# Kernel optimization log

Hardware: AMD Instinct MI355X
Metric: run time of the kernel (lower is better)

The kernel has to match this reference:

```python
import jax, jax.numpy as jnp
import numpy as np

N = 100000
F_IN = 512
HID = 16
N_CLS = 40
E = 3200000


def gcn_conv(x, W, b, src, dst, n_nodes):
    # PyG GCNConv: add self loops, symmetric deg^{-1/2} norm, linear, aggregate.
    loop = jnp.arange(n_nodes, dtype=src.dtype)
    s = jnp.concatenate([src, loop])  # [E+N]
    d = jnp.concatenate([dst, loop])
    deg = jax.ops.segment_sum(jnp.ones_like(d, dtype=x.dtype), d, num_segments=n_nodes)
    dinv = jnp.where(deg > 0, jax.lax.rsqrt(deg), 0.0)
    norm = dinv[s] * dinv[d]  # [E+N]
    h = x @ W  # [N, out] -- transform before propagate (cheaper: out <= in)
    msg = h[s] * norm[:, None]  # gather + scale
    out = jax.ops.segment_sum(msg, d, num_segments=n_nodes)  # scatter-add
    return out + b


def setup_inputs() -> dict:
    key = jax.random.key(0)
    ks = jax.random.split(key, 6)
    x = jax.random.normal(ks[0], (N, F_IN), dtype=jnp.float32)
    edge_index = jax.random.randint(ks[1], (2, E), 0, N, dtype=jnp.int64)
    W1 = jax.random.normal(ks[2], (F_IN, HID), dtype=jnp.float32) / np.sqrt(F_IN)
    b1 = jnp.zeros((HID,), dtype=jnp.float32)
    W2 = jax.random.normal(ks[3], (HID, N_CLS), dtype=jnp.float32) / np.sqrt(HID)
    b2 = jnp.zeros((N_CLS,), dtype=jnp.float32)
    return {"x": x, "edge_index": edge_index, "W1": W1, "b1": b1, "W2": W2, "b2": b2}


def reference(x, edge_index, W1, b1, W2, b2):
    src, dst = edge_index[0], edge_index[1]
    h = gcn_conv(x, W1, b1, src, dst, x.shape[0])
    h = jax.nn.relu(h)
    # dropout: eval mode (identity) for a deterministic reference
    h = gcn_conv(h, W2, b2, src, dst, x.shape[0])
    return jax.nn.log_softmax(h, axis=1)
```

## Files before the change

### kernel.cpp

```cpp
#include <hip/hip_runtime.h>

#define N_NODES 100000
#define NEDGE   3200000
#define F_IN    512
#define HID     16
#define NCLS    40

#define BSHIFT  8
#define BNODES  256
#define NBUCK   ((N_NODES + BNODES - 1) / BNODES)
#define BCAP    8832
#define EPB     5120
#define NPART   (NEDGE / EPB)
#define NGEMM   ((N_NODES + 63) / 64)

typedef __bf16 bf16x8 __attribute__((ext_vector_type(8)));
typedef float floatx4 __attribute__((ext_vector_type(4)));
typedef _Float16 f16x4 __attribute__((ext_vector_type(4)));

__global__ __launch_bounds__(256) void k_partgemm(
        const int* __restrict__ src, const int* __restrict__ dst,
        int* __restrict__ gcnt, int* __restrict__ ebuf,
        const float* __restrict__ x, const float* __restrict__ W1,
        _Float16* __restrict__ h1u) {
    __shared__ char smraw[32768];
    int t = threadIdx.x;

    if (blockIdx.x < NPART) {
        int* hist = (int*)smraw;
        for (int i = t; i < NBUCK; i += 256) hist[i] = 0;
        __syncthreads();

        int base = blockIdx.x * EPB + t * 4;
        int4 dr[5];
        #pragma unroll
        for (int s = 0; s < 5; s++) {
            dr[s] = *(const int4*)(dst + base + s * 1024);
            atomicAdd(&hist[dr[s].x >> BSHIFT], 1);
            atomicAdd(&hist[dr[s].y >> BSHIFT], 1);
            atomicAdd(&hist[dr[s].z >> BSHIFT], 1);
            atomicAdd(&hist[dr[s].w >> BSHIFT], 1);
        }
        __syncthreads();

        for (int i = t; i < NBUCK; i += 256) {
            int h = hist[i];
            hist[i] = h ? atomicAdd(&gcnt[i], h) : 0;
        }
        __syncthreads();

        #pragma unroll
        for (int s = 0; s < 5; s++) {
            int4 s4 = *(const int4*)(src + base + s * 1024);
            int dd[4] = {dr[s].x, dr[s].y, dr[s].z, dr[s].w};
            int ss[4] = {s4.x, s4.y, s4.z, s4.w};
            #pragma unroll
            for (int j = 0; j < 4; j++) {
                int d = dd[j];
                int b = d >> BSHIFT;
                int p = atomicAdd(&hist[b], 1);
                if (p < BCAP) ebuf[b * BCAP + p] = ((d & (BNODES - 1)) << 17) | ss[j];
            }
        }
    } else {
        __bf16* wh = (__bf16*)smraw;
        __bf16* wl = wh + 8192;
        for (int e = t; e < 8192; e += 256) {
            int c = e >> 9, l = (e >> 3) & 63, j = e & 7;
            int k = c * 32 + ((l >> 4) << 3) + j;
            int n = l & 15;
            float wv = W1[k * HID + n];
            __bf16 h = (__bf16)wv;
            wh[e] = h;
            wl[e] = (__bf16)(wv - (float)h);
        }
        __syncthreads();

        int wave = t >> 6, lane = t & 63;
        int q = lane >> 4, m = lane & 15;
        int row0 = (blockIdx.x - NPART) * 64 + wave * 16;
        int rowa = row0 + m;
        if (rowa >= N_NODES) rowa = N_NODES - 1;
        const float* xr = x + (size_t)rowa * F_IN + q * 8;

        floatx4 acc = {0.f, 0.f, 0.f, 0.f};
        #pragma unroll 4
        for (int c = 0; c < 16; c++) {
            float4 a0 = *(const float4*)(xr + c * 32);
            float4 a1 = *(const float4*)(xr + c * 32 + 4);
            float xv[8] = {a0.x, a0.y, a0.z, a0.w, a1.x, a1.y, a1.z, a1.w};
            bf16x8 ah, al;
            #pragma unroll
            for (int j = 0; j < 8; j++) {
                __bf16 h = (__bf16)xv[j];
                ah[j] = h;
                al[j] = (__bf16)(xv[j] - (float)h);
            }
            bf16x8 bh = *(const bf16x8*)&wh[(c * 64 + lane) * 8];
            bf16x8 bl = *(const bf16x8*)&wl[(c * 64 + lane) * 8];
            acc = __builtin_amdgcn_mfma_f32_16x16x32_bf16(ah, bh, acc, 0, 0, 0);
            acc = __builtin_amdgcn_mfma_f32_16x16x32_bf16(ah, bl, acc, 0, 0, 0);
            acc = __builtin_amdgcn_mfma_f32_16x16x32_bf16(al, bh, acc, 0, 0, 0);
        }
        #pragma unroll
        for (int r = 0; r < 4; r++) {
            int grow = row0 + q * 4 + r;
            if (grow < N_NODES)
                h1u[grow * HID + (lane & 15)] = (_Float16)acc[r];
        }
    }
}

__global__ __launch_bounds__(256) void k_sortb(const int* __restrict__ gcnt,
                                               const int* __restrict__ ebuf,
                                               int* __restrict__ col,
                                               int* __restrict__ rinfo,
                                               _Float16* __restrict__ h1) {
    __shared__ int ed[BCAP];
    __shared__ int cnt[BNODES];
    __shared__ int pref[BNODES];
    int b = blockIdx.x, t = threadIdx.x;

    int partial = 0;
    for (int i = t; i < b; i += 256) partial += gcnt[i];
    pref[t] = partial;
    __syncthreads();
    for (int off = 128; off; off >>= 1) {
        if (t < off) pref[t] += pref[t + off];
        __syncthreads();
    }
    int gbase = pref[0];
    __syncthreads();

    int ne = gcnt[b];
    if (ne > BCAP) ne = BCAP;
    cnt[t] = 0;
    __syncthreads();
    for (int i = t; i < ne; i += 256) {
        int e = ebuf[b * BCAP + i];
        ed[i] = e;
        atomicAdd(&cnt[e >> 17], 1);
    }
    __syncthreads();
    int c = cnt[t];
    pref[t] = c;
    __syncthreads();
    for (int off = 1; off < 256; off <<= 1) {
        int add = (t >= off) ? pref[t - off] : 0;
        __syncthreads();
        pref[t] += add;
        __syncthreads();
    }
    int start = pref[t] - c;
    int v = b * BNODES + t;
    if (v < N_NODES) {
        rinfo[v] = (c << 22) | (gbase + start);
        float dv = rsqrtf((float)(c + 1));
        f16x4* row = (f16x4*)(h1 + (size_t)v * HID);
        #pragma unroll
        for (int r = 0; r < 4; r++) {
            f16x4 vv = row[r];
            vv[0] = (_Float16)(dv * (float)vv[0]);
            vv[1] = (_Float16)(dv * (float)vv[1]);
            vv[2] = (_Float16)(dv * (float)vv[2]);
            vv[3] = (_Float16)(dv * (float)vv[3]);
            row[r] = vv;
        }
    }
    cnt[t] = start;
    __syncthreads();
    for (int i = t; i < ne; i += 256) {
        int e = ed[i];
        int pos = atomicAdd(&cnt[e >> 17], 1);
        col[gbase + pos] = e & 0x1FFFF;
    }
}

#define ACC4(gv) { a0 += (float)gv[0]; a1 += (float)gv[1]; \
                   a2 += (float)gv[2]; a3 += (float)gv[3]; }

__global__ __launch_bounds__(256) void k_agg1(const _Float16* __restrict__ h1s,
        const int* __restrict__ rinfo, const int* __restrict__ col,
        const float* __restrict__ b1, _Float16* __restrict__ ys) {
    int g = blockIdx.x * 256 + threadIdx.x;
    int v = g >> 2, q = g & 3;
    if (v >= N_NODES) return;
    int ri = rinfo[v];
    int beg = ri & 0x3FFFFF;
    int deg = (ri >> 22) & 0x3FF;
    int end = beg + deg;
    const f16x4* tab = (const f16x4*)h1s;
    float a0 = 0.f, a1 = 0.f, a2 = 0.f, a3 = 0.f;
    int j = beg;
    for (; j + 7 < end; j += 8) {
        int c0 = col[j],     c1 = col[j + 1], c2 = col[j + 2], c3 = col[j + 3];
        int c4 = col[j + 4], c5 = col[j + 5], c6 = col[j + 6], c7 = col[j + 7];
        f16x4 g0 = tab[c0 * 4 + q], g1 = tab[c1 * 4 + q];
        f16x4 g2 = tab[c2 * 4 + q], g3 = tab[c3 * 4 + q];
        f16x4 g4 = tab[c4 * 4 + q], g5 = tab[c5 * 4 + q];
        f16x4 g6 = tab[c6 * 4 + q], g7 = tab[c7 * 4 + q];
        ACC4(g0) ACC4(g1) ACC4(g2) ACC4(g3)
        ACC4(g4) ACC4(g5) ACC4(g6) ACC4(g7)
    }
    for (; j < end; j++) {
        f16x4 gv = tab[col[j] * 4 + q];
        ACC4(gv)
    }
    f16x4 sv = tab[v * 4 + q];
    ACC4(sv)
    float dv = rsqrtf((float)(deg + 1));
    f16x4 o;
    o[0] = (_Float16)(dv * fmaxf(dv * a0 + b1[q * 4 + 0], 0.f));
    o[1] = (_Float16)(dv * fmaxf(dv * a1 + b1[q * 4 + 1], 0.f));
    o[2] = (_Float16)(dv * fmaxf(dv * a2 + b1[q * 4 + 2], 0.f));
    o[3] = (_Float16)(dv * fmaxf(dv * a3 + b1[q * 4 + 3], 0.f));
    ((f16x4*)ys)[v * 4 + q] = o;
}

__global__ __launch_bounds__(256) void k_agg2(const _Float16* __restrict__ ys,
        const int* __restrict__ rinfo, const int* __restrict__ col,
        const float* __restrict__ W2, const float* __restrict__ b2,
        float* __restrict__ out) {
    __shared__ float w2s[HID * NCLS];
    __shared__ float b2s[NCLS];
    int t = threadIdx.x;
    for (int i = t; i < HID * NCLS; i += 256) w2s[i] = W2[i];
    if (t < NCLS) b2s[t] = b2[t];
    __syncthreads();

    int g = blockIdx.x * 256 + t;
    int v = g >> 2, q = g & 3;
    if (v >= N_NODES) return;
    int ri = rinfo[v];
    int beg = ri & 0x3FFFFF;
    int deg = (ri >> 22) & 0x3FF;
    int end = beg + deg;
    const f16x4* tab = (const f16x4*)ys;
    float a0 = 0.f, a1 = 0.f, a2 = 0.f, a3 = 0.f;
    int j = beg;
    for (; j + 7 < end; j += 8) {
        int c0 = col[j],     c1 = col[j + 1], c2 = col[j + 2], c3 = col[j + 3];
        int c4 = col[j + 4], c5 = col[j + 5], c6 = col[j + 6], c7 = col[j + 7];
        f16x4 g0 = tab[c0 * 4 + q], g1 = tab[c1 * 4 + q];
        f16x4 g2 = tab[c2 * 4 + q], g3 = tab[c3 * 4 + q];
        f16x4 g4 = tab[c4 * 4 + q], g5 = tab[c5 * 4 + q];
        f16x4 g6 = tab[c6 * 4 + q], g7 = tab[c7 * 4 + q];
        ACC4(g0) ACC4(g1) ACC4(g2) ACC4(g3)
        ACC4(g4) ACC4(g5) ACC4(g6) ACC4(g7)
    }
    for (; j < end; j++) {
        f16x4 gv = tab[col[j] * 4 + q];
        ACC4(gv)
    }
    f16x4 sv = tab[v * 4 + q];
    ACC4(sv)
    float dv = rsqrtf((float)(deg + 1));
    float tv[4] = {dv * a0, dv * a1, dv * a2, dv * a3};

    float lg[10];
    #pragma unroll
    for (int i = 0; i < 10; i++) lg[i] = b2s[q * 10 + i];
    #pragma unroll
    for (int k = 0; k < 16; k++) {
        float tk = __shfl(tv[k & 3], k >> 2, 4);
        #pragma unroll
        for (int i = 0; i < 10; i++)
            lg[i] = fmaf(tk, w2s[k * NCLS + q * 10 + i], lg[i]);
    }
    float mx = lg[0];
    #pragma unroll
    for (int i = 1; i < 10; i++) mx = fmaxf(mx, lg[i]);
    mx = fmaxf(mx, __shfl_xor(mx, 1, 4));
    mx = fmaxf(mx, __shfl_xor(mx, 2, 4));
    float s = 0.f;
    #pragma unroll
    for (int i = 0; i < 10; i++) s += __expf(lg[i] - mx);
    s += __shfl_xor(s, 1, 4);
    s += __shfl_xor(s, 2, 4);
    float lse = mx + __logf(s);
    #pragma unroll
    for (int i = 0; i < 10; i++) out[v * NCLS + q * 10 + i] = lg[i] - lse;
}

extern "C" void kernel_launch(void* const* d_in, const int* in_sizes, int n_in,
                              void* d_out, int out_size, void* d_ws, size_t ws_size,
                              hipStream_t stream) {
    const float* x  = (const float*)d_in[0];
    const int*   ei = (const int*)d_in[1];
    const float* W1 = (const float*)d_in[2];
    const float* b1 = (const float*)d_in[3];
    const float* W2 = (const float*)d_in[4];
    const float* b2 = (const float*)d_in[5];
    float* out = (float*)d_out;
    const int* src = ei;
    const int* dst = ei + NEDGE;

    char* w = (char*)d_ws;
    size_t o = 0;
    auto alloc = [&](size_t bytes) -> char* {
        char* p = w + o;
        o += (bytes + 511) & ~(size_t)511;
        return p;
    };
    int*      gcnt  = (int*)alloc((size_t)NBUCK * 4);
    int*      rinfo = (int*)alloc((size_t)N_NODES * 4);
    int*      col   = (int*)alloc((size_t)NEDGE * 4);
    int*      ebuf  = (int*)alloc((size_t)NBUCK * BCAP * 4);
    _Float16* h1s   = (_Float16*)alloc((size_t)N_NODES * HID * 2);
    _Float16* ys    = (_Float16*)alloc((size_t)N_NODES * HID * 2);

    hipMemsetAsync(gcnt, 0, (size_t)NBUCK * 4, stream);

    k_partgemm<<<NPART + NGEMM, 256, 0, stream>>>(src, dst, gcnt, ebuf, x, W1, h1s);
    k_sortb   <<<NBUCK, 256, 0, stream>>>(gcnt, ebuf, col, rinfo, h1s);
    k_agg1    <<<(N_NODES * 4 + 255) / 256, 256, 0, stream>>>(h1s, rinfo, col, b1, ys);
    k_agg2    <<<(N_NODES * 4 + 255) / 256, 256, 0, stream>>>(ys, rinfo, col, W2, b2, out);
}
```

Before: 431.3 us.

## Stage edge partition in shared memory for coalesced bucket writes

The partition blocks now compute a local exclusive prefix over bucket counts, scatter each edge into a shared-memory staging buffer grouped by bucket, and then write the staged edges out in order. Consecutive threads therefore write contiguous runs into each bucket's global region instead of scattering individual words randomly. The cost is a block-wide scan with many barriers, more shared memory per block (which may lower occupancy), and an extra pass over the staged data.

Measured after the change: 424.0 us. Within noise of the previous version (-1.7%).

```diff
diff --git a/kernel.cpp b/kernel.cpp
--- a/kernel.cpp
+++ b/kernel.cpp
@@ -23,11 +23,16 @@
         int* __restrict__ gcnt, int* __restrict__ ebuf,
         const float* __restrict__ x, const float* __restrict__ W1,
         _Float16* __restrict__ h1u) {
-    __shared__ char smraw[32768];
+    __shared__ char smraw[36864];
     int t = threadIdx.x;
 
     if (blockIdx.x < NPART) {
-        int* hist = (int*)smraw;
+        int* hist  = (int*)smraw;
+        int* lpref = hist + 512;
+        int* cur   = lpref + 512;
+        int* ed    = cur + 512;
+        unsigned short* abuf = (unsigned short*)(ed + EPB);
+
         for (int i = t; i < NBUCK; i += 256) hist[i] = 0;
         __syncthreads();
 
@@ -43,10 +48,32 @@
         }
         __syncthreads();
 
+        int c0 = 0, c1 = 0;
+        if (t < 196) {
+            c0 = hist[2 * t];
+            c1 = (2 * t + 1 < NBUCK) ? hist[2 * t + 1] : 0;
+        }
+        int sums = c0 + c1;
+        cur[t] = sums;
+        __syncthreads();
+        for (int off = 1; off < 256; off <<= 1) {
+            int add = (t >= off) ? cur[t - off] : 0;
+            __syncthreads();
+            cur[t] += add;
+            __syncthreads();
+        }
+        if (t < 196) {
+            int excl = cur[t] - sums;
+            lpref[2 * t] = excl;
+            if (2 * t + 1 < NBUCK) lpref[2 * t + 1] = excl + c0;
+        }
+        __syncthreads();
+
         for (int i = t; i < NBUCK; i += 256) {
-            int h = hist[i];
-            hist[i] = h ? atomicAdd(&gcnt[i], h) : 0;
-        }
+            int c = hist[i];
+            hist[i] = c ? atomicAdd(&gcnt[i], c) : 0;
+        }
+        for (int i = t; i < 512; i += 256) cur[i] = 0;
         __syncthreads();
 
         #pragma unroll
@@ -58,9 +85,18 @@
             for (int j = 0; j < 4; j++) {
                 int d = dd[j];
                 int b = d >> BSHIFT;
-                int p = atomicAdd(&hist[b], 1);
-                if (p < BCAP) ebuf[b * BCAP + p] = ((d & (BNODES - 1)) << 17) | ss[j];
+                int c = atomicAdd(&cur[b], 1);
+                int slot = lpref[b] + c;
+                ed[slot] = ((d & (BNODES - 1)) << 17) | ss[j];
+                abuf[slot] = (unsigned short)b;
             }
+        }
+        __syncthreads();
+
+        for (int i = t; i < EPB; i += 256) {
+            int b = abuf[i];
+            int off = hist[b] + (i - lpref[b]);
+            if (off < BCAP) ebuf[b * BCAP + off] = ed[i];
         }
     } else {
         __bf16* wh = (__bf16*)smraw;
```
